# Kernel optimization log

Measured on AMD Instinct MI355X. Metric: run time of the kernel, lower is better.

## Reference

```python
import jax, jax.numpy as jnp
import numpy as np

B, L, H = 32, 2048, 512


def setup_inputs() -> dict:
    key = jax.random.key(0)
    k1, k2, k3, k4, k5, k6 = jax.random.split(key, 6)
    scale = 1.0 / np.sqrt(H)
    return {
        "query": jax.random.normal(k1, (B, H), dtype=jnp.float32),
        "ref": jax.random.normal(k2, (B, L, H), dtype=jnp.float32),
        "mask": jax.random.randint(k3, (B, L), 0, 2) == 1,
        # learned params (torch Linear weight layout: [out, in]; apply as x @ W.T)
        "W_ref": jax.random.normal(k4, (H, H), dtype=jnp.float32) * scale,
        "W_q": jax.random.normal(k5, (H, H), dtype=jnp.float32) * scale,
        "v": jax.random.normal(k6, (H,), dtype=jnp.float32) * scale,
    }


def reference(query, ref, mask, W_ref, W_q, v):
    scale = 1.0 / np.sqrt(H)
    # additive (Bahdanau) scores: v^T tanh(W_ref ref + W_q q)
    encoded_ref = jnp.einsum("blh,oh->blo", ref, W_ref)          # (B, L, H)
    encoded_q = jnp.einsum("bh,oh->bo", query, W_q)[:, None, :]  # (B, 1, H)
    scores = jnp.einsum("blh,h->bl", jnp.tanh(encoded_ref + encoded_q), v)
    scores = scores * scale
    scores = jnp.where(mask, -1e9, scores)
    attn = jax.nn.softmax(scores, axis=1)                         # (B, L)
    glimpse = jnp.einsum("bl,blh->bh", attn, ref)                 # (B, H)
    return glimpse, scores
```

## Files before the change

### kernel.cpp

```cpp
#include <hip/hip_runtime.h>
#include <hip/hip_bf16.h>
#include <cstdint>

typedef __attribute__((ext_vector_type(4))) float f32x4;
typedef __attribute__((ext_vector_type(8))) short s16x8;

#define NB   32
#define NL   2048
#define NH   512
#define NM   (NB * NL)
#define SCALE 0.04419417382415922f

__device__ __forceinline__ ushort f2bf(float f) {
    __hip_bfloat16 b = __float2bfloat16(f);
    return *reinterpret_cast<ushort*>(&b);
}
__device__ __forceinline__ unsigned long long pack4(float4 f) {
    union { ushort u[4]; unsigned long long v; } p;
    p.u[0] = f2bf(f.x); p.u[1] = f2bf(f.y); p.u[2] = f2bf(f.z); p.u[3] = f2bf(f.w);
    return p.v;
}

#define GL16(g, l)                                                         \
    __builtin_amdgcn_global_load_lds(                                      \
        (const __attribute__((address_space(1))) unsigned int*)(g),        \
        (__attribute__((address_space(3))) unsigned int*)(l), 16, 0, 0)

__global__ __launch_bounds__(256) void k_pre(const float* __restrict__ W,
                                             ushort* __restrict__ Wb,
                                             const float* __restrict__ query,
                                             const float* __restrict__ Wq,
                                             float* __restrict__ eq) {
    int bid = blockIdx.x;
    int t = threadIdx.x;
    if (bid < 64) {
        const float4* F = (const float4*)W;
        unsigned long long* U = (unsigned long long*)Wb;
        int base = bid * 1024 + t;
        float4 f[4];
#pragma unroll
        for (int k = 0; k < 4; ++k) f[k] = F[base + k * 256];
#pragma unroll
        for (int k = 0; k < 4; ++k) U[base + k * 256] = pack4(f[k]);
    } else {
        __shared__ float q[NH];
        int b = bid - 64;
        q[t] = query[b * NH + t];
        q[t + 256] = query[b * NH + t + 256];
        __syncthreads();
#pragma unroll
        for (int half = 0; half < 2; ++half) {
            int o = t + half * 256;
            const float4* w = (const float4*)(Wq + (size_t)o * NH);
            float acc = 0.f;
#pragma unroll 4
            for (int i = 0; i < NH / 4; ++i) {
                float4 x = w[i];
                acc += q[4 * i] * x.x + q[4 * i + 1] * x.y + q[4 * i + 2] * x.z + q[4 * i + 3] * x.w;
            }
            eq[b * NH + o] = acc;
        }
    }
}

__global__ __launch_bounds__(256, 2) void k_gemm_full(const float* __restrict__ ref,
                                                      const ushort* __restrict__ Wb,
                                                      const float* __restrict__ eq,
                                                      const float* __restrict__ v,
                                                      const int* __restrict__ mask,
                                                      float* __restrict__ out_sc) {
    __shared__ char smem[81920];
    ushort* Bs0 = (ushort*)smem;
    ushort* Bs1 = (ushort*)(smem + 32768);
    float*  As0 = (float*)(smem + 65536);
    float*  As1 = (float*)(smem + 73728);

    int tid = threadIdx.x;
    int lane = tid & 63, wid = tid >> 6;
    int blk = blockIdx.x;
    int m0g = blk << 6;
    int b = blk >> 5;

    f32x4 acc[4][8];
#pragma unroll
    for (int i = 0; i < 4; ++i)
#pragma unroll
        for (int j = 0; j < 8; ++j) acc[i][j] = (f32x4)(0.f);

    const ushort* bglob = Wb + ((size_t)(wid * 128) + (lane >> 2)) * NH + ((lane & 3) << 3);
    const float* aglob = ref + (size_t)(m0g + wid * 16 + (lane >> 3)) * NH
                             + (((lane & 7) ^ ((lane >> 3) & 7)) << 2);

    int lr = lane & 15, kq = lane >> 4;
    int bbase = (wid * 128 + lr) * 32 + (kq << 3);
    int ac0 = (((2 * kq) ^ (lr & 7)) << 2);
    int ac1 = (((2 * kq + 1) ^ (lr & 7)) << 2);

#define STAGE(Bsb, Asb, kt)                                                \
    {   _Pragma("unroll")                                                  \
        for (int j = 0; j < 8; ++j)                                        \
            GL16(bglob + (kt) * 32 + j * 16 * NH,                          \
                 Bsb + (wid * 128 + j * 16) * 32);                         \
        GL16(aglob + (kt) * 32,          Asb + (wid * 16) * 32);           \
        GL16(aglob + (kt) * 32 + 8 * NH, Asb + (wid * 16 + 8) * 32); }

#define READ_CVT(Bsb, Asb)                                                       \
    _Pragma("unroll")                                                            \
    for (int f = 0; f < 8; ++f) bfr[f] = *(const s16x8*)&Bsb[bbase + f * 512];   \
    _Pragma("unroll")                                                            \
    for (int f = 0; f < 4; ++f) {                                                \
        float4 a0 = *(const float4*)(Asb + (f * 16 + lr) * 32 + ac0);            \
        float4 a1 = *(const float4*)(Asb + (f * 16 + lr) * 32 + ac1);            \
        union { ushort u[8]; s16x8 v; } p;                                       \
        p.u[0] = f2bf(a0.x); p.u[1] = f2bf(a0.y);                                \
        p.u[2] = f2bf(a0.z); p.u[3] = f2bf(a0.w);                                \
        p.u[4] = f2bf(a1.x); p.u[5] = f2bf(a1.y);                                \
        p.u[6] = f2bf(a1.z); p.u[7] = f2bf(a1.w);                                \
        af[f] = p.v;                                                             \
    }

#define MFMA_ALL()                                                               \
    __builtin_amdgcn_s_setprio(1);                                               \
    _Pragma("unroll")                                                            \
    for (int fr = 0; fr < 4; ++fr)                                               \
        _Pragma("unroll")                                                        \
        for (int fc = 0; fc < 8; ++fc)                                           \
            acc[fr][fc] = __builtin_amdgcn_mfma_f32_16x16x32_bf16(               \
                af[fr], bfr[fc], acc[fr][fc], 0, 0, 0);                          \
    __builtin_amdgcn_s_setprio(0);

    STAGE(Bs0, As0, 0)
    STAGE(Bs1, As1, 1)

#pragma unroll 1
    for (int t2 = 0; t2 < 7; ++t2) {
        {
            s16x8 bfr[8], af[4];
            asm volatile("s_waitcnt vmcnt(10)" ::: "memory");
            __builtin_amdgcn_s_barrier();
            READ_CVT(Bs0, As0)
            asm volatile("s_waitcnt lgkmcnt(0)" ::: "memory");
            __builtin_amdgcn_sched_barrier(0);
            __builtin_amdgcn_s_barrier();
            STAGE(Bs0, As0, 2 * t2 + 2)
            MFMA_ALL()
        }
        {
            s16x8 bfr[8], af[4];
            asm volatile("s_waitcnt vmcnt(10)" ::: "memory");
            __builtin_amdgcn_s_barrier();
            READ_CVT(Bs1, As1)
            asm volatile("s_waitcnt lgkmcnt(0)" ::: "memory");
            __builtin_amdgcn_sched_barrier(0);
            __builtin_amdgcn_s_barrier();
            STAGE(Bs1, As1, 2 * t2 + 3)
            MFMA_ALL()
        }
    }
    {
        s16x8 bfr[8], af[4];
        asm volatile("s_waitcnt vmcnt(10)" ::: "memory");
        __builtin_amdgcn_s_barrier();
        READ_CVT(Bs0, As0)
        MFMA_ALL()
    }
    {
        s16x8 bfr[8], af[4];
        asm volatile("s_waitcnt vmcnt(0)" ::: "memory");
        __builtin_amdgcn_s_barrier();
        READ_CVT(Bs1, As1)
        MFMA_ALL()
    }
#undef STAGE
#undef READ_CVT
#undef MFMA_ALL

    __syncthreads();

    float* sc_red = (float*)smem;
    const float* eqb = eq + b * NH;
    float vv[8], ee[8];
#pragma unroll
    for (int fc = 0; fc < 8; ++fc) {
        int c = wid * 128 + fc * 16 + lr;
        vv[fc] = v[c];
        ee[fc] = eqb[c];
    }
#pragma unroll
    for (int fr = 0; fr < 4; ++fr) {
#pragma unroll
        for (int reg = 0; reg < 4; ++reg) {
            float s = 0.f;
#pragma unroll
            for (int fc = 0; fc < 8; ++fc) {
                float x = acc[fr][fc][reg] + ee[fc];
                float t = 1.f - 2.f / (__expf(2.f * x) + 1.f);
                s += vv[fc] * t;
            }
            s += __shfl_xor(s, 1);
            s += __shfl_xor(s, 2);
            s += __shfl_xor(s, 4);
            s += __shfl_xor(s, 8);
            if (lr == 0) sc_red[wid * 64 + fr * 16 + kq * 4 + reg] = s;
        }
    }
    __syncthreads();
    if (tid < 64) {
        float t = 0.f;
#pragma unroll
        for (int w = 0; w < 4; ++w) t += sc_red[w * 64 + tid];
        t *= SCALE;
        int rg = m0g + tid;
        if (mask[rg] != 0) t = -1e9f;
        out_sc[rg] = t;
    }
}

__global__ __launch_bounds__(256) void k_smglp(const float* __restrict__ scores,
                                               const float* __restrict__ ref,
                                               float* __restrict__ glp) {
    int sp = blockIdx.x, b = blockIdx.y;
    int tid = threadIdx.x;
    int lane = tid & 63, wid = tid >> 6;
    __shared__ float red[4];
    __shared__ float asl[128];
    float sc[8];
    float mx = -3.4e38f;
#pragma unroll
    for (int i = 0; i < 8; ++i) {
        sc[i] = scores[b * NL + i * 256 + tid];
        mx = fmaxf(mx, sc[i]);
    }
#pragma unroll
    for (int o = 32; o >= 1; o >>= 1) mx = fmaxf(mx, __shfl_xor(mx, o));
    if (lane == 0) red[wid] = mx;
    __syncthreads();
    mx = fmaxf(fmaxf(red[0], red[1]), fmaxf(red[2], red[3]));
    __syncthreads();
    float ls = 0.f;
#pragma unroll
    for (int i = 0; i < 8; ++i) {
        float e = __expf(sc[i] - mx);
        ls += e;
        if (i == (sp >> 1) && (tid >> 7) == (sp & 1)) asl[tid & 127] = e;
    }
#pragma unroll
    for (int o = 32; o >= 1; o >>= 1) ls += __shfl_xor(ls, o);
    if (lane == 0) red[wid] = ls;
    __syncthreads();
    float inv = 1.f / (red[0] + red[1] + red[2] + red[3]);

    const float* rb = ref + ((size_t)b * NL + sp * 128) * NH;
    float2 acc = make_float2(0.f, 0.f);
#pragma unroll 4
    for (int l = 0; l < 128; ++l) {
        float a = asl[l];
        float2 r = ((const float2*)(rb + (size_t)l * NH))[tid];
        acc.x += a * r.x;
        acc.y += a * r.y;
    }
    acc.x *= inv;
    acc.y *= inv;
    ((float2*)(glp + (size_t)(sp * NB + b) * NH))[tid] = acc;
}

__global__ __launch_bounds__(256) void k_gred(const float* __restrict__ glp,
                                              float* __restrict__ out_gl) {
    int idx = blockIdx.x * 256 + threadIdx.x;
    float s = 0.f;
#pragma unroll
    for (int sp = 0; sp < 16; ++sp) s += glp[sp * (NB * NH) + idx];
    out_gl[idx] = s;
}

extern "C" void kernel_launch(void* const* d_in, const int* in_sizes, int n_in,
                              void* d_out, int out_size, void* d_ws, size_t ws_size,
                              hipStream_t stream) {
    const float* query = (const float*)d_in[0];
    const float* ref   = (const float*)d_in[1];
    const int*   mask  = (const int*)d_in[2];
    const float* W_ref = (const float*)d_in[3];
    const float* W_q   = (const float*)d_in[4];
    const float* v     = (const float*)d_in[5];

    float* out_gl = (float*)d_out;
    float* out_sc = out_gl + NB * NH;

    char* w = (char*)d_ws;
    ushort* wW = (ushort*)w;
    float* eq  = (float*)(w + 524288);
    float* glp = (float*)(w + 589824);

    k_pre<<<96, 256, 0, stream>>>(W_ref, wW, query, W_q, eq);
    k_gemm_full<<<1024, 256, 0, stream>>>(ref, wW, eq, v, mask, out_sc);
    k_smglp<<<dim3(16, NB), 256, 0, stream>>>(out_sc, ref, glp);
    k_gred<<<64, 256, 0, stream>>>(glp, out_gl);
}
```

Before: 120.6 us.

## Convert ref tile to bf16 on register load and store bf16 in LDS

The A operand (ref, fp32) was previously copied into LDS as fp32 via direct global-to-LDS loads, and every wave then read it and converted it to bf16 on each use. Now each thread loads its slice into registers, converts once, and writes packed bf16 into a swizzled LDS buffer one stage ahead. This roughly halves the LDS footprint and LDS read traffic for A and removes the redundant per-wave conversions. In exchange it adds register pressure, replaces async LDS loads with register round-trips, and needs more complex wait counts and swizzling on B.

```diff
diff --git a/kernel.cpp b/kernel.cpp
--- a/kernel.cpp
+++ b/kernel.cpp
@@ -69,11 +69,11 @@
                                                       const float* __restrict__ v,
                                                       const int* __restrict__ mask,
                                                       float* __restrict__ out_sc) {
-    __shared__ char smem[81920];
+    __shared__ char smem[73728];
     ushort* Bs0 = (ushort*)smem;
     ushort* Bs1 = (ushort*)(smem + 32768);
-    float*  As0 = (float*)(smem + 65536);
-    float*  As1 = (float*)(smem + 73728);
+    ushort* As0 = (ushort*)(smem + 65536);
+    ushort* As1 = (ushort*)(smem + 69632);
 
     int tid = threadIdx.x;
     int lane = tid & 63, wid = tid >> 6;
@@ -87,37 +87,41 @@
 #pragma unroll
         for (int j = 0; j < 8; ++j) acc[i][j] = (f32x4)(0.f);
 
-    const ushort* bglob = Wb + ((size_t)(wid * 128) + (lane >> 2)) * NH + ((lane & 3) << 3);
-    const float* aglob = ref + (size_t)(m0g + wid * 16 + (lane >> 3)) * NH
-                             + (((lane & 7) ^ ((lane >> 3) & 7)) << 2);
+    const ushort* bglob = Wb + ((size_t)(wid * 128) + (lane >> 2)) * NH
+                             + ((((lane & 3) ^ ((lane >> 2) & 3))) << 3);
+    int arow = tid >> 2, acl = tid & 3;
+    const float* aglob = ref + (size_t)(m0g + arow) * NH + acl * 8;
+    int awr = arow * 32 + ((acl ^ (arow & 3)) << 3);
 
     int lr = lane & 15, kq = lane >> 4;
-    int bbase = (wid * 128 + lr) * 32 + (kq << 3);
-    int ac0 = (((2 * kq) ^ (lr & 7)) << 2);
-    int ac1 = (((2 * kq + 1) ^ (lr & 7)) << 2);
-
-#define STAGE(Bsb, Asb, kt)                                                \
-    {   _Pragma("unroll")                                                  \
-        for (int j = 0; j < 8; ++j)                                        \
-            GL16(bglob + (kt) * 32 + j * 16 * NH,                          \
-                 Bsb + (wid * 128 + j * 16) * 32);                         \
-        GL16(aglob + (kt) * 32,          Asb + (wid * 16) * 32);           \
-        GL16(aglob + (kt) * 32 + 8 * NH, Asb + (wid * 16 + 8) * 32); }
-
-#define READ_CVT(Bsb, Asb)                                                       \
+    int bbase = (wid * 128 + lr) * 32 + ((kq ^ (lr & 3)) << 3);
+    int abase = lr * 32 + ((kq ^ (lr & 3)) << 3);
+
+    float4 qa0, qa1;
+
+#define LOAD_A(kt)                                              \
+    {   qa0 = *(const float4*)(aglob + (kt) * 32);              \
+        qa1 = *(const float4*)(aglob + (kt) * 32 + 4); }
+
+#define WRITE_A(Asb)                                            \
+    {   union { ushort u[8]; s16x8 v; } p;                      \
+        p.u[0] = f2bf(qa0.x); p.u[1] = f2bf(qa0.y);             \
+        p.u[2] = f2bf(qa0.z); p.u[3] = f2bf(qa0.w);             \
+        p.u[4] = f2bf(qa1.x); p.u[5] = f2bf(qa1.y);             \
+        p.u[6] = f2bf(qa1.z); p.u[7] = f2bf(qa1.w);             \
+        *(s16x8*)&(Asb)[awr] = p.v; }
+
+#define STAGE_B(Bsb, kt)                                        \
+    {   _Pragma("unroll")                                       \
+        for (int j = 0; j < 8; ++j)                             \
+            GL16(bglob + (kt) * 32 + j * 16 * NH,               \
+                 (Bsb) + (wid * 128 + j * 16) * 32); }
+
+#define READ_FRAGS(Bsb, Asb)                                                     \
     _Pragma("unroll")                                                            \
-    for (int f = 0; f < 8; ++f) bfr[f] = *(const s16x8*)&Bsb[bbase + f * 512];   \
+    for (int f = 0; f < 4; ++f) af[f] = *(const s16x8*)&(Asb)[abase + f * 512];  \
     _Pragma("unroll")                                                            \
-    for (int f = 0; f < 4; ++f) {                                                \
-        float4 a0 = *(const float4*)(Asb + (f * 16 + lr) * 32 + ac0);            \
-        float4 a1 = *(const float4*)(Asb + (f * 16 + lr) * 32 + ac1);            \
-        union { ushort u[8]; s16x8 v; } p;                                       \
-        p.u[0] = f2bf(a0.x); p.u[1] = f2bf(a0.y);                                \
-        p.u[2] = f2bf(a0.z); p.u[3] = f2bf(a0.w);                                \
-        p.u[4] = f2bf(a1.x); p.u[5] = f2bf(a1.y);                                \
-        p.u[6] = f2bf(a1.z); p.u[7] = f2bf(a1.w);                                \
-        af[f] = p.v;                                                             \
-    }
+    for (int f = 0; f < 8; ++f) bfr[f] = *(const s16x8*)&(Bsb)[bbase + f * 512];
 
 #define MFMA_ALL()                                                               \
     __builtin_amdgcn_s_setprio(1);                                               \
@@ -129,50 +133,74 @@
                 af[fr], bfr[fc], acc[fr][fc], 0, 0, 0);                          \
     __builtin_amdgcn_s_setprio(0);
 
-    STAGE(Bs0, As0, 0)
-    STAGE(Bs1, As1, 1)
+    LOAD_A(0)
+    float4 ra0 = qa0, ra1 = qa1;
+    LOAD_A(1)
+    STAGE_B(Bs0, 0)
+    STAGE_B(Bs1, 1)
+    asm volatile("s_waitcnt vmcnt(18)" ::: "memory");
+    {
+        union { ushort u[8]; s16x8 v; } p;
+        p.u[0] = f2bf(ra0.x); p.u[1] = f2bf(ra0.y);
+        p.u[2] = f2bf(ra0.z); p.u[3] = f2bf(ra0.w);
+        p.u[4] = f2bf(ra1.x); p.u[5] = f2bf(ra1.y);
+        p.u[6] = f2bf(ra1.z); p.u[7] = f2bf(ra1.w);
+        *(s16x8*)&As0[awr] = p.v;
+    }
+    asm volatile("s_waitcnt lgkmcnt(0)" ::: "memory");
+    __builtin_amdgcn_s_barrier();
 
 #pragma unroll 1
     for (int t2 = 0; t2 < 7; ++t2) {
         {
             s16x8 bfr[8], af[4];
-            asm volatile("s_waitcnt vmcnt(10)" ::: "memory");
+            asm volatile("s_waitcnt vmcnt(8)" ::: "memory");
             __builtin_amdgcn_s_barrier();
-            READ_CVT(Bs0, As0)
+            READ_FRAGS(Bs0, As0)
+            WRITE_A(As1)
             asm volatile("s_waitcnt lgkmcnt(0)" ::: "memory");
             __builtin_amdgcn_sched_barrier(0);
             __builtin_amdgcn_s_barrier();
-            STAGE(Bs0, As0, 2 * t2 + 2)
+            LOAD_A(2 * t2 + 2)
+            STAGE_B(Bs0, 2 * t2 + 2)
             MFMA_ALL()
         }
         {
             s16x8 bfr[8], af[4];
-            asm volatile("s_waitcnt vmcnt(10)" ::: "memory");
+            asm volatile("s_waitcnt vmcnt(8)" ::: "memory");
             __builtin_amdgcn_s_barrier();
-            READ_CVT(Bs1, As1)
+            READ_FRAGS(Bs1, As1)
+            WRITE_A(As0)
             asm volatile("s_waitcnt lgkmcnt(0)" ::: "memory");
             __builtin_amdgcn_sched_barrier(0);
             __builtin_amdgcn_s_barrier();
-            STAGE(Bs1, As1, 2 * t2 + 3)
+            LOAD_A(2 * t2 + 3)
+            STAGE_B(Bs1, 2 * t2 + 3)
             MFMA_ALL()
         }
     }
     {
         s16x8 bfr[8], af[4];
-        asm volatile("s_waitcnt vmcnt(10)" ::: "memory");
+        asm volatile("s_waitcnt vmcnt(8)" ::: "memory");
         __builtin_amdgcn_s_barrier();
-        READ_CVT(Bs0, As0)
+        READ_FRAGS(Bs0, As0)
+        WRITE_A(As1)
+        asm volatile("s_waitcnt lgkmcnt(0)" ::: "memory");
+        __builtin_amdgcn_sched_barrier(0);
+        __builtin_amdgcn_s_barrier();
         MFMA_ALL()
     }
     {
         s16x8 bfr[8], af[4];
         asm volatile("s_waitcnt vmcnt(0)" ::: "memory");
         __builtin_amdgcn_s_barrier();
-        READ_CVT(Bs1, As1)
+        READ_FRAGS(Bs1, As1)
         MFMA_ALL()
     }
-#undef STAGE
-#undef READ_CVT
+#undef LOAD_A
+#undef WRITE_A
+#undef STAGE_B
+#undef READ_FRAGS
 #undef MFMA_ALL
 
     __syncthreads();
```

After: 128.4 us. 1.07x slower.
